# Kernel tuning notes

Hardware: AMD Instinct MI355X
Metric: run time of the kernel (lower is better)

Reference implementation:

```python
import jax, jax.numpy as jnp
import numpy as np


def setup_inputs() -> dict:
    key = jax.random.key(0)
    k1, k2, k3 = jax.random.split(key, 3)
    B, Cin, H, W = 16, 128, 56, 56
    Cout, Kh, Kw = 256, 3, 3
    tensor = jax.random.normal(k1, (B, Cin, H, W), dtype=jnp.float32)
    weights = jax.random.normal(k2, (Cout, Cin, Kh, Kw), dtype=jnp.float32) * 0.05
    bias = jax.random.normal(k3, (Cout,), dtype=jnp.float32) * 0.05
    return {"tensor": tensor, "weights": weights, "bias": bias}


def reference(tensor, weights, bias):
    # OpticalConvolution: unfold (im2col) -> per-output-channel augmented dot
    # products (w . patch + b). Mathematically this is a standard 2D conv with
    # bias, expressed here as one fused conv instead of a per-channel loop.
    stride, padding, dilation = (1, 1), ((1, 1), (1, 1)), (1, 1)
    out = jax.lax.conv_general_dilated(
        tensor, weights,
        window_strides=stride,
        padding=padding,
        rhs_dilation=dilation,
        dimension_numbers=("NCHW", "OIHW", "NCHW"),
    )
    return out + bias[None, :, None, None]  # [B, Cout, H_out, W_out]
```

## Files before the change

kernel.cpp:

```cpp
#include <hip/hip_runtime.h>

typedef unsigned short ushort_t;
typedef unsigned int uint_t;

#define CIN   128
#define COUT  256
#define HH    56
#define WW    56
#define HWSZ  3136
#define BATCH 16
#define NPIX  50176
#define KTOT  1152

typedef __attribute__((ext_vector_type(8))) short bf16x8;
typedef __attribute__((ext_vector_type(4))) float f32x4;

__device__ __forceinline__ ushort_t f2bf(float v) {
    union { float f; uint_t u; } c; c.f = v;
    uint_t u = c.u;
    u += 0x7FFFu + ((u >> 16) & 1u);
    return (ushort_t)(u >> 16);
}

__global__ __launch_bounds__(256) void prep(
    const float* __restrict__ tensor, const float* __restrict__ weights,
    ushort_t* __restrict__ Ib, ushort_t* __restrict__ Wt, ushort_t* __restrict__ guard)
{
    __shared__ ushort_t lds[8704];
    const int tid = threadIdx.x;

    if (blockIdx.x < 784) {
        int t   = blockIdx.x;
        int b   = t / 49;
        int hwt = t - b * 49;
        int hw0 = hwt * 64;
        const float* src = tensor + (size_t)b * CIN * HWSZ + hw0;
        for (int k = 0; k < 8; ++k) {
            int f  = tid + k * 256;
            int ci = f >> 4;
            int ho = (f & 15) * 4;
            float4 v = *(const float4*)(src + (size_t)ci * HWSZ + ho);
            lds[(ho + 0) * 136 + ci] = f2bf(v.x);
            lds[(ho + 1) * 136 + ci] = f2bf(v.y);
            lds[(ho + 2) * 136 + ci] = f2bf(v.z);
            lds[(ho + 3) * 136 + ci] = f2bf(v.w);
        }
        __syncthreads();
        ushort_t* dst = Ib + ((size_t)b * HWSZ + hw0) * CIN;
        for (int k = 0; k < 4; ++k) {
            int s   = tid + k * 256;
            int ho  = s >> 4;
            int cio = (s & 15) * 8;
            bf16x8 v = *(const bf16x8*)&lds[ho * 136 + cio];
            *(bf16x8*)(dst + ho * 128 + cio) = v;
        }
    } else {
        int co = blockIdx.x - 784;
        const float* src = weights + (size_t)co * KTOT;
        for (int k = 0; k < 5; ++k) {
            int idx = tid + k * 256;
            if (idx < KTOT) {
                int ci  = idx / 9;
                int pos = idx - ci * 9;
                lds[pos * 128 + ci] = f2bf(src[idx]);
            }
        }
        __syncthreads();
        ushort_t* dst = Wt + (size_t)co * KTOT;
        for (int k = 0; k < 5; ++k) {
            int idx = tid + k * 256;
            if (idx < KTOT) dst[idx] = lds[idx];
        }
        if (blockIdx.x == 784 && tid < 8) guard[tid] = 0;
    }
}

__global__ __launch_bounds__(256, 4) void conv_gemm(
    const ushort_t* __restrict__ Wt,
    const ushort_t* __restrict__ Ib,
    const float* __restrict__ bias,
    float* __restrict__ out,
    const ushort_t* __restrict__ guard)
{
    __shared__ ushort_t A_lds[2 * 128 * 32];
    __shared__ ushort_t B_lds[2 * 128 * 32];

    const int tid  = threadIdx.x;
    const int wave = tid >> 6;
    const int lane = tid & 63;
    const int quad = lane >> 4;
    const int l16  = lane & 15;

    const int bm = blockIdx.x & 1;
    const int bn = blockIdx.x >> 1;

    const int wm = (wave >> 1) * 64;
    const int wn = (wave & 1) * 64;

    const ushort_t* aBase[2];
    const ushort_t* pb0[2];
    int py[2], px[2];
    for (int q = 0; q < 2; ++q) {
        int slot = wave * 128 + q * 64 + lane;
        int r = slot >> 2, c = slot & 3;
        aBase[q] = Wt + (size_t)(bm * 128 + r) * KTOT + c * 8;
        int pix = bn * 128 + r;
        int b_  = pix / HWSZ;
        int rem = pix - b_ * HWSZ;
        int y_  = rem / WW;
        int x_  = rem - y_ * WW;
        py[q] = y_; px[q] = x_;
        pb0[q] = Ib + (size_t)pix * CIN + c * 8;
    }
    const int ldsOff = (wave * 128) * 8;

    const f32x4 zero = {0.f, 0.f, 0.f, 0.f};
    f32x4 acc[4][4];
    for (int i = 0; i < 4; ++i)
        for (int j = 0; j < 4; ++j) acc[i][j] = zero;

    for (int pos = 0; pos < 9; ++pos) {
        const int dy = pos / 3 - 1;
        const int dx = pos - (pos / 3) * 3 - 1;
        const ushort_t* bp[2];
        bool okq[2];
        for (int q = 0; q < 2; ++q) {
            int yy = py[q] + dy, xx = px[q] + dx;
            okq[q] = ((uint_t)yy < (uint_t)HH) && ((uint_t)xx < (uint_t)WW);
            bp[q]  = pb0[q] + (dy * WW + dx) * CIN;
        }
        for (int cc2 = 0; cc2 < 2; ++cc2) {
            for (int p = 0; p < 2; ++p) {
                const int cc = cc2 * 2 + p;
                for (int q = 0; q < 2; ++q) {
                    __builtin_amdgcn_global_load_lds(
                        (const __attribute__((address_space(1))) void*)(aBase[q] + pos * 128 + cc * 32),
                        (__attribute__((address_space(3))) void*)(&A_lds[p * 4096 + ldsOff + q * 512]),
                        16, 0, 0);
                }
                for (int q = 0; q < 2; ++q) {
                    const ushort_t* g = okq[q] ? (bp[q] + cc * 32) : guard;
                    __builtin_amdgcn_global_load_lds(
                        (const __attribute__((address_space(1))) void*)g,
                        (__attribute__((address_space(3))) void*)(&B_lds[p * 4096 + ldsOff + q * 512]),
                        16, 0, 0);
                }
            }
            __syncthreads();
            for (int p = 0; p < 2; ++p) {
                bf16x8 af[4], bfr[4];
                for (int i = 0; i < 4; ++i)
                    af[i] = *(const bf16x8*)&A_lds[p * 4096 + (wm + i * 16 + l16) * 32 + quad * 8];
                for (int j = 0; j < 4; ++j)
                    bfr[j] = *(const bf16x8*)&B_lds[p * 4096 + (wn + j * 16 + l16) * 32 + quad * 8];
                for (int i = 0; i < 4; ++i)
                    for (int j = 0; j < 4; ++j)
                        acc[i][j] = __builtin_amdgcn_mfma_f32_16x16x32_bf16(
                            af[i], bfr[j], acc[i][j], 0, 0, 0);
            }
            __syncthreads();
        }
    }

    int obase[4];
    for (int j = 0; j < 4; ++j) {
        int pix = bn * 128 + wn + j * 16 + l16;
        int b_  = pix / HWSZ;
        int rem = pix - b_ * HWSZ;
        obase[j] = b_ * (COUT * HWSZ) + rem;
    }
    for (int i = 0; i < 4; ++i) {
        for (int r = 0; r < 4; ++r) {
            int co = bm * 128 + wm + i * 16 + quad * 4 + r;
            float bv = bias[co];
            int coOff = co * HWSZ;
            for (int j = 0; j < 4; ++j) {
                out[(size_t)(obase[j] + coOff)] = acc[i][j][r] + bv;
            }
        }
    }
}

__global__ void naive_conv(const float* __restrict__ in, const float* __restrict__ w,
                           const float* __restrict__ bias, float* __restrict__ out, int total) {
    int idx = blockIdx.x * 256 + threadIdx.x;
    if (idx >= total) return;
    int x = idx % WW; int t = idx / WW;
    int y = t % HH; t /= HH;
    int co = t % COUT; int b = t / COUT;
    float s = bias[co];
    const float* wr = w + (size_t)co * KTOT;
    for (int ci = 0; ci < CIN; ++ci) {
        const float* ir = in + (size_t)(b * CIN + ci) * HWSZ;
        for (int kh = 0; kh < 3; ++kh) {
            int yy = y + kh - 1;
            if ((uint_t)yy >= (uint_t)HH) continue;
            for (int kw = 0; kw < 3; ++kw) {
                int xx = x + kw - 1;
                if ((uint_t)xx >= (uint_t)WW) continue;
                s += ir[yy * WW + xx] * wr[ci * 9 + kh * 3 + kw];
            }
        }
    }
    out[idx] = s;
}

extern "C" void kernel_launch(void* const* d_in, const int* in_sizes, int n_in,
                              void* d_out, int out_size, void* d_ws, size_t ws_size,
                              hipStream_t stream) {
    const float* tensor  = (const float*)d_in[0];
    const float* weights = (const float*)d_in[1];
    const float* bias    = (const float*)d_in[2];
    float* out = (float*)d_out;

    const size_t GUARD    = 1024;
    const size_t WT_BYTES = (size_t)COUT * KTOT * 2;
    const size_t IB_BYTES = (size_t)NPIX * CIN * 2;
    const size_t NEED     = GUARD + WT_BYTES + IB_BYTES;

    if (ws_size >= NEED) {
        ushort_t* guard = (ushort_t*)d_ws;
        ushort_t* Wt    = (ushort_t*)((char*)d_ws + GUARD);
        ushort_t* Ib    = (ushort_t*)((char*)d_ws + GUARD + WT_BYTES);
        prep<<<784 + COUT, 256, 0, stream>>>(tensor, weights, Ib, Wt, guard);
        conv_gemm<<<(COUT / 128) * (NPIX / 128), 256, 0, stream>>>(Wt, Ib, bias, out, guard);
    } else {
        int total = BATCH * COUT * HWSZ;
        naive_conv<<<(total + 255) / 256, 256, 0, stream>>>(tensor, weights, bias, out, total);
    }
}
```

Measured before the change: 134.8 us.

## Double-buffer conv GEMM K-stages with XOR-swizzled LDS and packed prep conversion

Replaces the two-chunks-then-sync loop with a 36-stage double-buffered pipeline: the next stage's global-to-LDS loads are issued while MFMAs run on the current buffer, so each stage needs only one barrier. It XOR-swizzles the LDS column chunk for the A and B tiles to cut bank conflicts on fragment reads. The prep kernel now packs two channels per bf16x2 conversion into 32-bit LDS words with a swizzle, and the occupancy hint is dropped from launch_bounds. The one-barrier scheme depends on the global_load_lds writes being complete at the barrier (no explicit vmcnt wait is visible), and register pressure may rise without the occupancy hint.

```diff
diff --git a/kernel.cpp b/kernel.cpp
--- a/kernel.cpp
+++ b/kernel.cpp
@@ -1,4 +1,5 @@
 #include <hip/hip_runtime.h>
+#include <hip/hip_bf16.h>
 
 typedef unsigned short ushort_t;
 typedef unsigned int uint_t;
@@ -22,11 +23,17 @@
     return (ushort_t)(u >> 16);
 }
 
+__device__ __forceinline__ uint_t pk2bf(float lo, float hi) {
+    __hip_bfloat162 h = __float22bfloat162_rn(make_float2(lo, hi));
+    union { __hip_bfloat162 h; uint_t u; } c; c.h = h;
+    return c.u;
+}
+
 __global__ __launch_bounds__(256) void prep(
     const float* __restrict__ tensor, const float* __restrict__ weights,
     ushort_t* __restrict__ Ib, ushort_t* __restrict__ Wt, ushort_t* __restrict__ guard)
 {
-    __shared__ ushort_t lds[8704];
+    __shared__ __align__(16) uint_t lds_u[64 * 68];
     const int tid = threadIdx.x;
 
     if (blockIdx.x < 784) {
@@ -35,55 +42,67 @@
         int hwt = t - b * 49;
         int hw0 = hwt * 64;
         const float* src = tensor + (size_t)b * CIN * HWSZ + hw0;
-        for (int k = 0; k < 8; ++k) {
-            int f  = tid + k * 256;
-            int ci = f >> 4;
-            int ho = (f & 15) * 4;
-            float4 v = *(const float4*)(src + (size_t)ci * HWSZ + ho);
-            lds[(ho + 0) * 136 + ci] = f2bf(v.x);
-            lds[(ho + 1) * 136 + ci] = f2bf(v.y);
-            lds[(ho + 2) * 136 + ci] = f2bf(v.z);
-            lds[(ho + 3) * 136 + ci] = f2bf(v.w);
+        for (int k = 0; k < 4; ++k) {
+            int t2 = tid + k * 256;
+            int hb = t2 & 15;
+            int cp = t2 >> 4;
+            const float* s0 = src + (size_t)(2 * cp) * HWSZ + hb * 4;
+            float4 a  = *(const float4*)s0;
+            float4 bb = *(const float4*)(s0 + HWSZ);
+            uint_t w0 = pk2bf(a.x, bb.x);
+            uint_t w1 = pk2bf(a.y, bb.y);
+            uint_t w2 = pk2bf(a.z, bb.z);
+            uint_t w3 = pk2bf(a.w, bb.w);
+            int c16  = cp >> 2;
+            int lb   = cp & 3;
+            int c16p = c16 ^ (hb & 7);
+            uint_t* base = &lds_u[(hb * 4) * 68 + c16p * 4 + lb];
+            base[0 * 68] = w0;
+            base[1 * 68] = w1;
+            base[2 * 68] = w2;
+            base[3 * 68] = w3;
         }
         __syncthreads();
         ushort_t* dst = Ib + ((size_t)b * HWSZ + hw0) * CIN;
         for (int k = 0; k < 4; ++k) {
-            int s   = tid + k * 256;
-            int ho  = s >> 4;
-            int cio = (s & 15) * 8;
-            bf16x8 v = *(const bf16x8*)&lds[ho * 136 + cio];
-            *(bf16x8*)(dst + ho * 128 + cio) = v;
+            int s2  = tid + k * 256;
+            int ho  = s2 >> 4;
+            int c16 = s2 & 15;
+            int c16p = c16 ^ ((ho >> 2) & 7);
+            uint4 v = *(const uint4*)&lds_u[ho * 68 + c16p * 4];
+            *(uint4*)(dst + ho * 128 + c16 * 8) = v;
         }
     } else {
         int co = blockIdx.x - 784;
+        ushort_t* lds_s = (ushort_t*)lds_u;
         const float* src = weights + (size_t)co * KTOT;
         for (int k = 0; k < 5; ++k) {
             int idx = tid + k * 256;
             if (idx < KTOT) {
                 int ci  = idx / 9;
                 int pos = idx - ci * 9;
-                lds[pos * 128 + ci] = f2bf(src[idx]);
+                lds_s[pos * 128 + ci] = f2bf(src[idx]);
             }
         }
         __syncthreads();
         ushort_t* dst = Wt + (size_t)co * KTOT;
         for (int k = 0; k < 5; ++k) {
             int idx = tid + k * 256;
-            if (idx < KTOT) dst[idx] = lds[idx];
+            if (idx < KTOT) dst[idx] = lds_s[idx];
         }
         if (blockIdx.x == 784 && tid < 8) guard[tid] = 0;
     }
 }
 
-__global__ __launch_bounds__(256, 4) void conv_gemm(
+__global__ __launch_bounds__(256) void conv_gemm(
     const ushort_t* __restrict__ Wt,
     const ushort_t* __restrict__ Ib,
     const float* __restrict__ bias,
     float* __restrict__ out,
     const ushort_t* __restrict__ guard)
 {
-    __shared__ ushort_t A_lds[2 * 128 * 32];
-    __shared__ ushort_t B_lds[2 * 128 * 32];
+    __shared__ ushort_t A_lds[2][128 * 32];
+    __shared__ ushort_t B_lds[2][128 * 32];
 
     const int tid  = threadIdx.x;
     const int wave = tid >> 6;
@@ -97,69 +116,69 @@
     const int wm = (wave >> 1) * 64;
     const int wn = (wave & 1) * 64;
 
-    const ushort_t* aBase[2];
-    const ushort_t* pb0[2];
+    const ushort_t* aCh[2];
+    const ushort_t* pbCh[2];
     int py[2], px[2];
     for (int q = 0; q < 2; ++q) {
         int slot = wave * 128 + q * 64 + lane;
-        int r = slot >> 2, c = slot & 3;
-        aBase[q] = Wt + (size_t)(bm * 128 + r) * KTOT + c * 8;
+        int r  = slot >> 2;
+        int c  = slot & 3;
+        int cF = c ^ ((r >> 1) & 3);
+        aCh[q] = Wt + (size_t)(bm * 128 + r) * KTOT + cF * 8;
         int pix = bn * 128 + r;
         int b_  = pix / HWSZ;
         int rem = pix - b_ * HWSZ;
         int y_  = rem / WW;
         int x_  = rem - y_ * WW;
         py[q] = y_; px[q] = x_;
-        pb0[q] = Ib + (size_t)pix * CIN + c * 8;
+        pbCh[q] = Ib + (size_t)pix * CIN + cF * 8;
     }
     const int ldsOff = (wave * 128) * 8;
+    const int xorc   = (l16 >> 1) & 3;
 
     const f32x4 zero = {0.f, 0.f, 0.f, 0.f};
     f32x4 acc[4][4];
     for (int i = 0; i < 4; ++i)
         for (int j = 0; j < 4; ++j) acc[i][j] = zero;
 
-    for (int pos = 0; pos < 9; ++pos) {
-        const int dy = pos / 3 - 1;
-        const int dx = pos - (pos / 3) * 3 - 1;
-        const ushort_t* bp[2];
-        bool okq[2];
+    auto stage = [&](int s, int buf) {
+        int pos = s >> 2;
+        int cc  = s & 3;
+        int p3  = pos / 3;
+        int dy  = p3 - 1;
+        int dx  = pos - p3 * 3 - 1;
+        int shift = (dy * WW + dx) * CIN;
+        for (int q = 0; q < 2; ++q) {
+            __builtin_amdgcn_global_load_lds(
+                (const __attribute__((address_space(1))) void*)(aCh[q] + pos * 128 + cc * 32),
+                (__attribute__((address_space(3))) void*)(&A_lds[buf][ldsOff + q * 512]),
+                16, 0, 0);
+        }
         for (int q = 0; q < 2; ++q) {
             int yy = py[q] + dy, xx = px[q] + dx;
-            okq[q] = ((uint_t)yy < (uint_t)HH) && ((uint_t)xx < (uint_t)WW);
-            bp[q]  = pb0[q] + (dy * WW + dx) * CIN;
-        }
-        for (int cc2 = 0; cc2 < 2; ++cc2) {
-            for (int p = 0; p < 2; ++p) {
-                const int cc = cc2 * 2 + p;
-                for (int q = 0; q < 2; ++q) {
-                    __builtin_amdgcn_global_load_lds(
-                        (const __attribute__((address_space(1))) void*)(aBase[q] + pos * 128 + cc * 32),
-                        (__attribute__((address_space(3))) void*)(&A_lds[p * 4096 + ldsOff + q * 512]),
-                        16, 0, 0);
-                }
-                for (int q = 0; q < 2; ++q) {
-                    const ushort_t* g = okq[q] ? (bp[q] + cc * 32) : guard;
-                    __builtin_amdgcn_global_load_lds(
-                        (const __attribute__((address_space(1))) void*)g,
-                        (__attribute__((address_space(3))) void*)(&B_lds[p * 4096 + ldsOff + q * 512]),
-                        16, 0, 0);
-                }
-            }
-            __syncthreads();
-            for (int p = 0; p < 2; ++p) {
-                bf16x8 af[4], bfr[4];
-                for (int i = 0; i < 4; ++i)
-                    af[i] = *(const bf16x8*)&A_lds[p * 4096 + (wm + i * 16 + l16) * 32 + quad * 8];
-                for (int j = 0; j < 4; ++j)
-                    bfr[j] = *(const bf16x8*)&B_lds[p * 4096 + (wn + j * 16 + l16) * 32 + quad * 8];
-                for (int i = 0; i < 4; ++i)
-                    for (int j = 0; j < 4; ++j)
-                        acc[i][j] = __builtin_amdgcn_mfma_f32_16x16x32_bf16(
-                            af[i], bfr[j], acc[i][j], 0, 0, 0);
-            }
-            __syncthreads();
-        }
+            bool ok = ((uint_t)yy < (uint_t)HH) && ((uint_t)xx < (uint_t)WW);
+            const ushort_t* g = ok ? (pbCh[q] + shift + cc * 32) : guard;
+            __builtin_amdgcn_global_load_lds(
+                (const __attribute__((address_space(1))) void*)g,
+                (__attribute__((address_space(3))) void*)(&B_lds[buf][ldsOff + q * 512]),
+                16, 0, 0);
+        }
+    };
+
+    stage(0, 0);
+    for (int s = 0; s < 36; ++s) {
+        __syncthreads();
+        if (s < 35) stage(s + 1, (s + 1) & 1);
+        const int p = s & 1;
+        bf16x8 af[4], bfr[4];
+        for (int i = 0; i < 4; ++i)
+            af[i] = *(const bf16x8*)&A_lds[p][(wm + i * 16 + l16) * 32 + (quad ^ xorc) * 8];
+        for (int j = 0; j < 4; ++j)
+            bfr[j] = *(const bf16x8*)&B_lds[p][(wn + j * 16 + l16) * 32 + (quad ^ xorc) * 8];
+        for (int i = 0; i < 4; ++i)
+            for (int j = 0; j < 4; ++j)
+                acc[i][j] = __builtin_amdgcn_mfma_f32_16x16x32_bf16(
+                    af[i], bfr[j], acc[i][j], 0, 0, 0);
     }
 
     int obase[4];
```

Result: slower. 147.3 us (+9.2%).
